# Kernel tuning notes

Hardware: AMD Instinct MI355X
Metric: run time of the kernel (lower is better)

Reference implementation:

```python
import jax, jax.numpy as jnp
import numpy as np

B, E, D, T, R = 8192, 4096, 256, 128, 4
K = 64                # dkn_n_neighbors
TAU_SQ = 4.0          # tau**2
EMB_SCALE = 0.07      # keeps sq-dists ~2.5 so exp(-d2) weights are meaningful
LOG_BASE = -27.6310211159
EPS = 1e-12


def _rev_cumsum(a, axis):
    # flip -> cumsum -> flip, as in torch .flip().cumsum().flip()
    return jnp.flip(jnp.cumsum(jnp.flip(a, axis), axis), axis)


def _kernel_weights(x, ex):
    # exact KNN stand-in for the ANN index: squared L2 distances [B, E]
    d2 = (jnp.sum(x * x, axis=1, keepdims=True)
          + jnp.sum(ex * ex, axis=1)[None, :]
          - 2.0 * (x @ ex.T))
    neg_d2, idx = jax.lax.top_k(-d2, K)          # k nearest per query
    sq = jnp.maximum(-neg_d2, 0.0)               # [B, K]
    vals = jnp.exp(-sq) * (sq <= TAU_SQ).astype(x.dtype)
    rows = jnp.arange(x.shape[0])[:, None]       # [B, 1]
    # sparse exp-distance weights scattered into dense [B, E]
    return jnp.zeros((x.shape[0], ex.shape[0]), x.dtype).at[rows, idx].set(vals)


def setup_inputs() -> dict:
    key = jax.random.key(0)
    k0, k1, k2, k3 = jax.random.split(key, 4)
    x = jax.random.normal(k0, (B, D), dtype=jnp.float32) * EMB_SCALE
    ex = jax.random.normal(k1, (E, D), dtype=jnp.float32) * EMB_SCALE
    log_ev = jax.random.normal(k2, (E, T, R), dtype=jnp.float32) - 2.0
    log_cen = jax.random.normal(k3, (E, T), dtype=jnp.float32) - 2.0
    log_b_ev = jnp.full((T, R), LOG_BASE, dtype=jnp.float32)
    log_b_cen = jnp.full((T,), LOG_BASE, dtype=jnp.float32)
    return {
        "x": x,
        "exemplar_embeddings": ex,
        "log_exemplar_event_counts": log_ev,
        "log_exemplar_censor_counts": log_cen,
        "log_baseline_event_counts": log_b_ev,
        "log_baseline_censor_counts": log_b_cen,
    }


def reference(x, exemplar_embeddings, log_exemplar_event_counts,
              log_exemplar_censor_counts, log_baseline_event_counts,
              log_baseline_censor_counts):
    kw = _kernel_weights(x, exemplar_embeddings)             # [B, E]

    b_ev = jnp.exp(log_baseline_event_counts)                # [T, R]
    b_cen = jnp.exp(log_baseline_censor_counts)              # [T]
    b_at_risk = _rev_cumsum(b_ev.sum(1) + b_cen, 0)          # [T]

    ev = jnp.exp(log_exemplar_event_counts)                  # [E, T, R]
    cen = jnp.exp(log_exemplar_censor_counts)                # [E, T]
    at_risk = _rev_cumsum(ev.sum(2) + cen, 1)                # [E, T]

    denom = kw @ at_risk + b_at_risk[None, :] + EPS          # [B, T]
    numer = jnp.einsum('be,etr->btr', kw, ev) + b_ev[None]   # [B, T, R]

    esh = jnp.clip(numer / denom[..., None], EPS, 1.0 - EPS) # [B, T, R]
    event_specific_hazards = jnp.moveaxis(esh, -1, 0)        # [R, B, T]
    overall = jnp.clip(numer.sum(-1) / denom, EPS, 1.0 - EPS)  # [B, T]
    return event_specific_hazards, overall
```

## Files before the change

### kernel.cpp

```cpp
#include <hip/hip_runtime.h>
#include <hip/hip_fp16.h>
#include <math.h>

namespace {

constexpr int NB = 8192;
constexpr int NE = 4096;
constexpr int ND = 256;
constexpr int NT = 128;
constexpr int NR = 4;
constexpr int NK = 64;
constexpr int NCAND = 320;
constexpr float TAUSQ = 4.0f;
constexpr float FEPS = 1e-12f;
constexpr float QS = 256.0f / 4.5f;

typedef short s16x8 __attribute__((ext_vector_type(8)));
typedef float f32x4 __attribute__((ext_vector_type(4)));

__device__ __forceinline__ unsigned short f2bf_rne(float f) {
  unsigned int u = __float_as_uint(f);
  unsigned int r = (u + 0x7FFFu + ((u >> 16) & 1u)) >> 16;
  return (unsigned short)r;
}
__device__ __forceinline__ unsigned short f2h(float f) {
  return __half_as_ushort(__float2half(f));
}
__device__ __forceinline__ float h2f(unsigned short s) {
  return __half2float(__ushort_as_half(s));
}

__device__ __forceinline__ void gl_lds16(const void* g, void* lds) {
  __builtin_amdgcn_global_load_lds(
      (const __attribute__((address_space(1))) unsigned int*)g,
      (__attribute__((address_space(3))) unsigned int*)lds, 16, 0, 0);
}

__global__ void k_prep(const float* __restrict__ lev, const float* __restrict__ lcen,
                       const float* __restrict__ lbev, const float* __restrict__ lbcen,
                       unsigned short* __restrict__ EVh, unsigned short* __restrict__ ARh,
                       float* __restrict__ bev, float* __restrict__ bar) {
  __shared__ float wtot;
  int t = threadIdx.x, l = t & 63;
  int e = blockIdx.x;
  float acc;
  if (e < NE) {
    acc = expf(lcen[(size_t)e * NT + t]);
    const float* src = lev + ((size_t)e * NT + t) * NR;
    float o0 = expf(src[0]), o1 = expf(src[1]), o2 = expf(src[2]), o3 = expf(src[3]);
    ushort4 h4;
    h4.x = f2h(o0); h4.y = f2h(o1); h4.z = f2h(o2); h4.w = f2h(o3);
    *reinterpret_cast<ushort4*>(EVh + ((size_t)e * NT + t) * NR) = h4;
    acc += o0 + o1 + o2 + o3;
  } else {
    acc = expf(lbcen[t]);
    const float* src = lbev + t * NR;
    float o0 = expf(src[0]), o1 = expf(src[1]), o2 = expf(src[2]), o3 = expf(src[3]);
    bev[t * NR + 0] = o0; bev[t * NR + 1] = o1;
    bev[t * NR + 2] = o2; bev[t * NR + 3] = o3;
    acc += o0 + o1 + o2 + o3;
  }
  float v = acc;
  #pragma unroll
  for (int o = 1; o < 64; o <<= 1) {
    float u = __shfl_down(v, o);
    if (l + o < 64) v += u;
  }
  if (t == 64) wtot = v;
  __syncthreads();
  if (t < 64) v += wtot;
  if (e < NE) ARh[(size_t)e * NT + t] = f2h(v);
  else        bar[t] = v;
}

__global__ void k_split(const float* __restrict__ x, const float* __restrict__ ex,
                        unsigned short* __restrict__ xh, unsigned short* __restrict__ eh,
                        float* __restrict__ xn, float* __restrict__ exn) {
  int row = blockIdx.x, l = threadIdx.x;
  bool isx = row < NB;
  const float* p = isx ? (x + (size_t)row * ND) : (ex + (size_t)(row - NB) * ND);
  unsigned short* dst = isx ? (xh + (size_t)row * ND) : (eh + (size_t)(row - NB) * ND);
  float4 v = reinterpret_cast<const float4*>(p)[l];
  float nv = v.x * v.x + v.y * v.y + v.z * v.z + v.w * v.w;
  ushort4 h4;
  h4.x = f2bf_rne(v.x); h4.y = f2bf_rne(v.y);
  h4.z = f2bf_rne(v.z); h4.w = f2bf_rne(v.w);
  reinterpret_cast<ushort4*>(dst)[l] = h4;
  for (int o = 32; o > 0; o >>= 1) nv += __shfl_down(nv, o);
  if (l == 0) { if (isx) xn[row] = nv; else exn[row - NB] = nv; }
}

__global__ __launch_bounds__(256) void k_dist_mfma(
    const unsigned short* __restrict__ xh, const unsigned short* __restrict__ eh,
    const float* __restrict__ xn, const float* __restrict__ exn,
    unsigned char* __restrict__ d2q) {
  __shared__ __align__(16) unsigned char As[128 * 128];
  __shared__ __align__(16) unsigned char Bs[128 * 128];
  int tid = threadIdx.x;
  int l = tid & 63, w = tid >> 6;
  int wr = w >> 1, wc = w & 1;

  int lid = blockIdx.x;
  int sl = (lid & 7) * 256 + (lid >> 3);
  int nb = (sl & 31) * 128;
  int mb = (sl >> 5) * 128;

  f32x4 acc[4][4];
  #pragma unroll
  for (int m = 0; m < 4; ++m)
    #pragma unroll
    for (int n = 0; n < 4; ++n)
      acc[m][n] = (f32x4){0.f, 0.f, 0.f, 0.f};

  for (int k0 = 0; k0 < ND; k0 += 64) {
    #pragma unroll
    for (int h = 0; h < 4; ++h) {
      int c = h * 256 + tid;
      int row = c >> 3, slot = c & 7;
      int swz = (row ^ (row >> 3)) & 7;
      int gcol = k0 + ((slot ^ swz) << 3);
      gl_lds16(xh + (size_t)(mb + row) * ND + gcol, As + c * 16);
      gl_lds16(eh + (size_t)(nb + row) * ND + gcol, Bs + c * 16);
    }
    __syncthreads();
    #pragma unroll
    for (int kk = 0; kk < 2; ++kk) {
      s16x8 af[4], bf_[4];
      int sl0 = kk * 4 + (l >> 4);
      #pragma unroll
      for (int m = 0; m < 4; ++m) {
        int r = wr * 64 + m * 16 + (l & 15);
        int swz = (r ^ (r >> 3)) & 7;
        af[m] = *(const s16x8*)(As + r * 128 + ((sl0 ^ swz) << 4));
      }
      #pragma unroll
      for (int n = 0; n < 4; ++n) {
        int r = wc * 64 + n * 16 + (l & 15);
        int swz = (r ^ (r >> 3)) & 7;
        bf_[n] = *(const s16x8*)(Bs + r * 128 + ((sl0 ^ swz) << 4));
      }
      #pragma unroll
      for (int m = 0; m < 4; ++m)
        #pragma unroll
        for (int n = 0; n < 4; ++n)
          acc[m][n] = __builtin_amdgcn_mfma_f32_16x16x32_bf16(af[m], bf_[n], acc[m][n], 0, 0, 0);
    }
    __syncthreads();
  }

  int col0 = nb + wc * 64 + (l & 15);
  int row0 = mb + wr * 64 + (l >> 4) * 4;
  float exnv[4];
  #pragma unroll
  for (int n = 0; n < 4; ++n) exnv[n] = exn[col0 + n * 16];
  #pragma unroll
  for (int m = 0; m < 4; ++m) {
    #pragma unroll
    for (int j = 0; j < 4; ++j) {
      int qrow = row0 + m * 16 + j;
      float xq = xn[qrow];
      #pragma unroll
      for (int n = 0; n < 4; ++n) {
        float d2 = xq + exnv[n] - 2.f * acc[m][n][j];
        int bin = (int)floorf(d2 * QS);
        bin = bin < 0 ? 0 : (bin > 255 ? 255 : bin);
        d2q[(size_t)qrow * NE + (col0 + n * 16)] = (unsigned char)bin;
      }
    }
  }
}

__global__ __launch_bounds__(256, 8) void k_select(
    const unsigned char* __restrict__ d2q,
    const float* __restrict__ x, const float* __restrict__ ex,
    const float* __restrict__ xn, const float* __restrict__ exn,
    float* __restrict__ selw, int* __restrict__ seli) {
  __shared__ unsigned int hist[256];
  __shared__ float4 xs[64];
  __shared__ int cand_e[NCAND];
  __shared__ float cand_d[NCAND];
  __shared__ unsigned int wsum[4];
  __shared__ int s_cb, s_nc;

  int tid = threadIdx.x;
  int l = tid & 63, w = tid >> 6;
  int b = blockIdx.x;

  uint4 rb = reinterpret_cast<const uint4*>(d2q + (size_t)b * NE)[tid];
  if (tid < 64) xs[tid] = reinterpret_cast<const float4*>(x + (size_t)b * ND)[tid];
  hist[tid] = 0u;
  __syncthreads();

  unsigned int wd[4] = {rb.x, rb.y, rb.z, rb.w};
  #pragma unroll
  for (int c = 0; c < 4; ++c)
    #pragma unroll
    for (int k = 0; k < 4; ++k)
      atomicAdd(&hist[(wd[c] >> (8 * k)) & 255u], 1u);

  int g = tid >> 4, gj = tid & 15;
  float4 xr0 = xs[gj], xr1 = xs[gj + 16], xr2 = xs[gj + 32], xr3 = xs[gj + 48];
  __syncthreads();

  if (w == 0) {
    unsigned int h0 = hist[l * 4], h1 = hist[l * 4 + 1], h2 = hist[l * 4 + 2], h3 = hist[l * 4 + 3];
    unsigned int gs = h0 + h1 + h2 + h3;
    unsigned int sc = gs;
    #pragma unroll
    for (int o = 1; o < 64; o <<= 1) { unsigned int v = __shfl_up(sc, o); if (l >= o) sc += v; }
    unsigned int excl = sc - gs;
    unsigned int c0 = excl + h0, c1 = c0 + h1, c2 = c1 + h2, c3 = c2 + h3;
    int local = (c0 >= (unsigned)NK) ? 0 : (c1 >= (unsigned)NK) ? 1
              : (c2 >= (unsigned)NK) ? 2 : (c3 >= (unsigned)NK) ? 3 : -1;
    unsigned long long ball = __ballot(local >= 0);
    int first = __ffsll((long long)ball) - 1;
    if (l == first) s_cb = l * 4 + local;
  }
  __syncthreads();
  int cbg = s_cb < 255 ? s_cb + 1 : 255;

  int myc = 0;
  #pragma unroll
  for (int c = 0; c < 4; ++c)
    #pragma unroll
    for (int k = 0; k < 4; ++k)
      myc += ((int)((wd[c] >> (8 * k)) & 255u) <= cbg) ? 1 : 0;
  int sc = myc;
  #pragma unroll
  for (int o = 1; o < 64; o <<= 1) { int v = __shfl_up(sc, o); if (l >= o) sc += v; }
  if (l == 63) wsum[w] = (unsigned)sc;
  __syncthreads();
  int base = 0;
  for (int i = 0; i < w; ++i) base += (int)wsum[i];
  int slot = base + sc - myc;
  #pragma unroll
  for (int c = 0; c < 4; ++c)
    #pragma unroll
    for (int k = 0; k < 4; ++k) {
      int bin = (int)((wd[c] >> (8 * k)) & 255u);
      if (bin <= cbg) {
        if (slot < NCAND) cand_e[slot] = tid * 16 + c * 4 + k;
        ++slot;
      }
    }
  if (tid == 255) s_nc = (base + sc) < NCAND ? (base + sc) : NCAND;
  __syncthreads();

  int nc = s_nc;
  float bxn = xn[b];
  for (int c = g; c < nc; c += 32) {
    int eA = cand_e[c];
    int has2 = (c + 16) < nc;
    int eB = has2 ? cand_e[c + 16] : eA;
    const float4* pA = reinterpret_cast<const float4*>(ex + (size_t)eA * ND);
    const float4* pB = reinterpret_cast<const float4*>(ex + (size_t)eB * ND);
    float4 a0 = pA[gj], a1 = pA[gj + 16], a2 = pA[gj + 32], a3 = pA[gj + 48];
    float4 b0 = pB[gj], b1 = pB[gj + 16], b2 = pB[gj + 32], b3 = pB[gj + 48];
    float sA = xr0.x * a0.x + xr0.y * a0.y + xr0.z * a0.z + xr0.w * a0.w
             + xr1.x * a1.x + xr1.y * a1.y + xr1.z * a1.z + xr1.w * a1.w
             + xr2.x * a2.x + xr2.y * a2.y + xr2.z * a2.z + xr2.w * a2.w
             + xr3.x * a3.x + xr3.y * a3.y + xr3.z * a3.z + xr3.w * a3.w;
    float sB = xr0.x * b0.x + xr0.y * b0.y + xr0.z * b0.z + xr0.w * b0.w
             + xr1.x * b1.x + xr1.y * b1.y + xr1.z * b1.z + xr1.w * b1.w
             + xr2.x * b2.x + xr2.y * b2.y + xr2.z * b2.z + xr2.w * b2.w
             + xr3.x * b3.x + xr3.y * b3.y + xr3.z * b3.z + xr3.w * b3.w;
    #pragma unroll
    for (int o = 1; o < 16; o <<= 1) {
      sA += __shfl_xor(sA, o, 16);
      sB += __shfl_xor(sB, o, 16);
    }
    if (gj == 0) {
      cand_d[c] = bxn + exn[eA] - 2.f * sA;
      if (has2) cand_d[c + 16] = bxn + exn[eB] - 2.f * sB;
    }
  }
  __syncthreads();

  for (int i = tid; i < nc; i += 256) {
    float di = cand_d[i];
    int rank = 0;
    for (int j = 0; j < nc; ++j) {
      float dj = cand_d[j];
      rank += (dj < di) || (dj == di && j < i);
    }
    if (rank < NK) {
      float sq = fmaxf(di, 0.f);
      float wgt = (sq <= TAUSQ) ? expf(-sq) : 0.f;
      selw[(size_t)b * NK + rank] = wgt;
      seli[(size_t)b * NK + rank] = cand_e[i];
    }
  }
  if (tid >= nc && tid < NK) {
    selw[(size_t)b * NK + tid] = 0.f;
    seli[(size_t)b * NK + tid] = 0;
  }
}

__global__ __launch_bounds__(256) void k_out(
    const unsigned short* __restrict__ EVh, const unsigned short* __restrict__ ARh,
    const float* __restrict__ bev, const float* __restrict__ bar,
    const float* __restrict__ selw, const int* __restrict__ seli,
    float* __restrict__ out) {
  __shared__ float wl[NK];
  __shared__ int il[NK];
  __shared__ float snum[NT * NR];
  __shared__ float sden[NT];
  int tid = threadIdx.x;
  int b = blockIdx.x;
  if (tid < NK) { wl[tid] = selw[(size_t)b * NK + tid]; il[tid] = seli[(size_t)b * NK + tid]; }
  __syncthreads();

  int g = tid >> 7;
  int t = tid & 127;
  float acc0 = 0.f, acc1 = 0.f, acc2 = 0.f, acc3 = 0.f, dacc = 0.f;
  for (int k = g; k < NK; k += 2) {
    float wgt = wl[k];
    int e = il[k];
    ushort4 v = reinterpret_cast<const ushort4*>(EVh + (size_t)e * (NT * NR))[t];
    acc0 += wgt * h2f(v.x);
    acc1 += wgt * h2f(v.y);
    acc2 += wgt * h2f(v.z);
    acc3 += wgt * h2f(v.w);
    dacc += wgt * h2f(ARh[(size_t)e * NT + t]);
  }
  if (g == 0) {
    snum[t * 4 + 0] = acc0; snum[t * 4 + 1] = acc1;
    snum[t * 4 + 2] = acc2; snum[t * 4 + 3] = acc3;
    sden[t] = dacc;
  }
  __syncthreads();
  if (g == 1) {
    snum[t * 4 + 0] += acc0 + bev[t * 4 + 0];
    snum[t * 4 + 1] += acc1 + bev[t * 4 + 1];
    snum[t * 4 + 2] += acc2 + bev[t * 4 + 2];
    snum[t * 4 + 3] += acc3 + bev[t * 4 + 3];
    sden[t] += dacc + bar[t] + FEPS;
  }
  __syncthreads();

  const float lo = FEPS, hi = 1.0f - FEPS;
  {
    int f = tid;
    int tt = f >> 2, r = f & 3;
    float h = snum[f] / sden[tt];
    h = fminf(fmaxf(h, lo), hi);
    out[((size_t)r * NB + b) * NT + tt] = h;
    int f1 = tid + 256;
    int t1 = f1 >> 2, r1 = f1 & 3;
    float h1 = snum[f1] / sden[t1];
    h1 = fminf(fmaxf(h1, lo), hi);
    out[((size_t)r1 * NB + b) * NT + t1] = h1;
  }
  if (tid < NT) {
    float sum = snum[4 * tid] + snum[4 * tid + 1] + snum[4 * tid + 2] + snum[4 * tid + 3];
    float ov = sum / sden[tid];
    ov = fminf(fmaxf(ov, lo), hi);
    out[(size_t)4 * NB * NT + (size_t)b * NT + tid] = ov;
  }
}

}

extern "C" void kernel_launch(void* const* d_in, const int* in_sizes, int n_in,
                              void* d_out, int out_size, void* d_ws, size_t ws_size,
                              hipStream_t stream) {
  (void)in_sizes; (void)n_in; (void)out_size; (void)ws_size;
  const float* x     = (const float*)d_in[0];
  const float* ex    = (const float*)d_in[1];
  const float* lev   = (const float*)d_in[2];
  const float* lcen  = (const float*)d_in[3];
  const float* lbev  = (const float*)d_in[4];
  const float* lbcen = (const float*)d_in[5];
  float* out = (float*)d_out;

  char* ws = (char*)d_ws;
  unsigned short* EVh = (unsigned short*)(ws);
  unsigned short* ARh = (unsigned short*)(ws + (4ull << 20));
  float* bev = (float*)(ws + (5ull << 20));
  float* bar = (float*)(ws + (5ull << 20) + 4096);
  float* exn = (float*)(ws + (5ull << 20) + 8192);
  float* xn  = (float*)(ws + (5ull << 20) + 8192 + (16u << 10));
  unsigned char* d2q = (unsigned char*)(ws + (6ull << 20));
  float* selw = (float*)(ws + (38ull << 20));
  int*   seli = (int*)  (ws + (40ull << 20));
  unsigned short* xh = (unsigned short*)(ws + (42ull << 20));
  unsigned short* eh = (unsigned short*)(ws + (46ull << 20));

  k_prep<<<NE + 1, NT, 0, stream>>>(lev, lcen, lbev, lbcen, EVh, ARh, bev, bar);
  k_split<<<NB + NE, 64, 0, stream>>>(x, ex, xh, eh, xn, exn);
  k_dist_mfma<<<2048, 256, 0, stream>>>(xh, eh, xn, exn, d2q);
  k_select<<<NB, 256, 0, stream>>>(d2q, x, ex, xn, exn, selw, seli);
  k_out<<<NB, 256, 0, stream>>>(EVh, ARh, bev, bar, selw, seli, out);
}
```

Baseline: 213.0 us.

## Merge split kernel into prep and replace full rank sort with window-based selection

Merges the bf16 split/norm kernel into the prep kernel as extra blocks, removing one launch. In k_select, the O(nc^2) rank computation over all candidates is replaced. Candidates clearly below the quantization threshold window are accepted via an atomic counter, and only candidates near the cutoff bin are rank-compared to fill the remaining slots. Output order becomes unsorted, which is fine for the scatter-style consumer. It assumes the quantized bin bounds hold and caps the ambiguous set at 128.

```diff
diff --git a/kernel.cpp b/kernel.cpp
--- a/kernel.cpp
+++ b/kernel.cpp
@@ -14,6 +14,7 @@
 constexpr float TAUSQ = 4.0f;
 constexpr float FEPS = 1e-12f;
 constexpr float QS = 256.0f / 4.5f;
+constexpr float HBIN = 4.5f / 256.f;
 
 typedef short s16x8 __attribute__((ext_vector_type(8)));
 typedef float f32x4 __attribute__((ext_vector_type(4)));
@@ -39,10 +40,31 @@
 __global__ void k_prep(const float* __restrict__ lev, const float* __restrict__ lcen,
                        const float* __restrict__ lbev, const float* __restrict__ lbcen,
                        unsigned short* __restrict__ EVh, unsigned short* __restrict__ ARh,
-                       float* __restrict__ bev, float* __restrict__ bar) {
+                       float* __restrict__ bev, float* __restrict__ bar,
+                       const float* __restrict__ x, const float* __restrict__ ex,
+                       unsigned short* __restrict__ xh, unsigned short* __restrict__ eh,
+                       float* __restrict__ xn, float* __restrict__ exn) {
   __shared__ float wtot;
   int t = threadIdx.x, l = t & 63;
-  int e = blockIdx.x;
+  int bid = blockIdx.x;
+
+  if (bid > NE) {
+    int r2 = (bid - (NE + 1)) * 2 + (t >> 6);
+    bool isx = r2 < NB;
+    const float* p = isx ? (x + (size_t)r2 * ND) : (ex + (size_t)(r2 - NB) * ND);
+    unsigned short* dst = isx ? (xh + (size_t)r2 * ND) : (eh + (size_t)(r2 - NB) * ND);
+    float4 v = reinterpret_cast<const float4*>(p)[l];
+    float nv = v.x * v.x + v.y * v.y + v.z * v.z + v.w * v.w;
+    ushort4 h4;
+    h4.x = f2bf_rne(v.x); h4.y = f2bf_rne(v.y);
+    h4.z = f2bf_rne(v.z); h4.w = f2bf_rne(v.w);
+    reinterpret_cast<ushort4*>(dst)[l] = h4;
+    for (int o = 32; o > 0; o >>= 1) nv += __shfl_down(nv, o);
+    if (l == 0) { if (isx) xn[r2] = nv; else exn[r2 - NB] = nv; }
+    return;
+  }
+
+  int e = bid;
   float acc;
   if (e < NE) {
     acc = expf(lcen[(size_t)e * NT + t]);
@@ -71,23 +93,6 @@
   if (t < 64) v += wtot;
   if (e < NE) ARh[(size_t)e * NT + t] = f2h(v);
   else        bar[t] = v;
-}
-
-__global__ void k_split(const float* __restrict__ x, const float* __restrict__ ex,
-                        unsigned short* __restrict__ xh, unsigned short* __restrict__ eh,
-                        float* __restrict__ xn, float* __restrict__ exn) {
-  int row = blockIdx.x, l = threadIdx.x;
-  bool isx = row < NB;
-  const float* p = isx ? (x + (size_t)row * ND) : (ex + (size_t)(row - NB) * ND);
-  unsigned short* dst = isx ? (xh + (size_t)row * ND) : (eh + (size_t)(row - NB) * ND);
-  float4 v = reinterpret_cast<const float4*>(p)[l];
-  float nv = v.x * v.x + v.y * v.y + v.z * v.z + v.w * v.w;
-  ushort4 h4;
-  h4.x = f2bf_rne(v.x); h4.y = f2bf_rne(v.y);
-  h4.z = f2bf_rne(v.z); h4.w = f2bf_rne(v.w);
-  reinterpret_cast<ushort4*>(dst)[l] = h4;
-  for (int o = 32; o > 0; o >>= 1) nv += __shfl_down(nv, o);
-  if (l == 0) { if (isx) xn[row] = nv; else exn[row - NB] = nv; }
 }
 
 __global__ __launch_bounds__(256) void k_dist_mfma(
@@ -181,6 +186,10 @@
   __shared__ float cand_d[NCAND];
   __shared__ unsigned int wsum[4];
   __shared__ int s_cb, s_nc;
+  __shared__ int s_m1, s_amb, s_out;
+  __shared__ int amb_ci[128];
+  __shared__ float amb_dv[128];
+  __shared__ unsigned char amb_ok[128];
 
   int tid = threadIdx.x;
   int l = tid & 63, w = tid >> 6;
@@ -189,6 +198,7 @@
   uint4 rb = reinterpret_cast<const uint4*>(d2q + (size_t)b * NE)[tid];
   if (tid < 64) xs[tid] = reinterpret_cast<const float4*>(x + (size_t)b * ND)[tid];
   hist[tid] = 0u;
+  if (tid == 0) { s_m1 = 0; s_amb = 0; s_out = 0; }
   __syncthreads();
 
   unsigned int wd[4] = {rb.x, rb.y, rb.z, rb.w};
@@ -217,7 +227,8 @@
     if (l == first) s_cb = l * 4 + local;
   }
   __syncthreads();
-  int cbg = s_cb < 255 ? s_cb + 1 : 255;
+  int cb = s_cb;
+  int cbg = cb < 255 ? cb + 1 : 255;
 
   int myc = 0;
   #pragma unroll
@@ -244,6 +255,7 @@
       }
     }
   if (tid == 255) s_nc = (base + sc) < NCAND ? (base + sc) : NCAND;
+  if (tid < NK) { selw[(size_t)b * NK + tid] = 0.f; seli[(size_t)b * NK + tid] = 0; }
   __syncthreads();
 
   int nc = s_nc;
@@ -276,23 +288,54 @@
   }
   __syncthreads();
 
+  float wlo = cb * HBIN - 0.5f * HBIN;
+  float whi = (cb + 1) * HBIN + 0.5f * HBIN;
+
   for (int i = tid; i < nc; i += 256) {
-    float di = cand_d[i];
-    int rank = 0;
-    for (int j = 0; j < nc; ++j) {
-      float dj = cand_d[j];
-      rank += (dj < di) || (dj == di && j < i);
-    }
-    if (rank < NK) {
-      float sq = fmaxf(di, 0.f);
-      float wgt = (sq <= TAUSQ) ? expf(-sq) : 0.f;
-      selw[(size_t)b * NK + rank] = wgt;
-      seli[(size_t)b * NK + rank] = cand_e[i];
-    }
-  }
-  if (tid >= nc && tid < NK) {
-    selw[(size_t)b * NK + tid] = 0.f;
-    seli[(size_t)b * NK + tid] = 0;
+    float d = cand_d[i];
+    if (d < wlo) {
+      atomicAdd(&s_m1, 1);
+    } else if (d <= whi) {
+      int p = atomicAdd(&s_amb, 1);
+      if (p < 128) { amb_ci[p] = i; amb_dv[p] = d; }
+    }
+  }
+  __syncthreads();
+  int m1 = s_m1;
+  int na = s_amb < 128 ? s_amb : 128;
+  int need = NK - m1;
+
+  if (tid < na) {
+    float di = amb_dv[tid];
+    int ci = amb_ci[tid];
+    int r = 0;
+    for (int j = 0; j < na; ++j) {
+      float dj = amb_dv[j];
+      r += (dj < di) || (dj == di && amb_ci[j] < ci);
+    }
+    amb_ok[tid] = (r < need) ? 1 : 0;
+  }
+  __syncthreads();
+
+  for (int i = tid; i < nc; i += 256) {
+    float d = cand_d[i];
+    if (d < wlo) {
+      int p = atomicAdd(&s_out, 1);
+      if (p < NK) {
+        float sq = fmaxf(d, 0.f);
+        selw[(size_t)b * NK + p] = (sq <= TAUSQ) ? expf(-sq) : 0.f;
+        seli[(size_t)b * NK + p] = cand_e[i];
+      }
+    }
+  }
+  if (tid < na && amb_ok[tid]) {
+    int p = atomicAdd(&s_out, 1);
+    if (p < NK) {
+      float d = amb_dv[tid];
+      float sq = fmaxf(d, 0.f);
+      selw[(size_t)b * NK + p] = (sq <= TAUSQ) ? expf(-sq) : 0.f;
+      seli[(size_t)b * NK + p] = cand_e[amb_ci[tid]];
+    }
   }
 }
 
@@ -386,8 +429,8 @@
   unsigned short* xh = (unsigned short*)(ws + (42ull << 20));
   unsigned short* eh = (unsigned short*)(ws + (46ull << 20));
 
-  k_prep<<<NE + 1, NT, 0, stream>>>(lev, lcen, lbev, lbcen, EVh, ARh, bev, bar);
-  k_split<<<NB + NE, 64, 0, stream>>>(x, ex, xh, eh, xn, exn);
+  k_prep<<<(NE + 1) + (NB + NE) / 2, NT, 0, stream>>>(
+      lev, lcen, lbev, lbcen, EVh, ARh, bev, bar, x, ex, xh, eh, xn, exn);
   k_dist_mfma<<<2048, 256, 0, stream>>>(xh, eh, xn, exn, d2q);
   k_select<<<NB, 256, 0, stream>>>(d2q, x, ex, xn, exn, selw, seli);
   k_out<<<NB, 256, 0, stream>>>(EVh, ARh, bev, bar, selw, seli, out);
```

Result: slower. 222.6 us (+4.5%).

## Merge prep and split kernels; split selection into histogram and rerank kernels

Applied to the files above, without the earlier changes.

Folds the bf16 split/norm work into the prep kernel launch, processing two rows per 128-thread block, which removes one kernel launch. It also splits the select kernel into two: one builds the histogram and writes candidate lists to global memory, the other reranks candidates with exact fp32 distances. This lowers per-kernel register and LDS use and so may raise occupancy, at the cost of an extra launch and a global round trip for the candidate lists.

```diff
diff --git a/kernel.cpp b/kernel.cpp
--- a/kernel.cpp
+++ b/kernel.cpp
@@ -39,10 +39,31 @@
 __global__ void k_prep(const float* __restrict__ lev, const float* __restrict__ lcen,
                        const float* __restrict__ lbev, const float* __restrict__ lbcen,
                        unsigned short* __restrict__ EVh, unsigned short* __restrict__ ARh,
-                       float* __restrict__ bev, float* __restrict__ bar) {
+                       float* __restrict__ bev, float* __restrict__ bar,
+                       const float* __restrict__ x, const float* __restrict__ ex,
+                       unsigned short* __restrict__ xh, unsigned short* __restrict__ eh,
+                       float* __restrict__ xn, float* __restrict__ exn) {
   __shared__ float wtot;
   int t = threadIdx.x, l = t & 63;
-  int e = blockIdx.x;
+  int bid = blockIdx.x;
+
+  if (bid > NE) {
+    int r2 = (bid - (NE + 1)) * 2 + (t >> 6);
+    bool isx = r2 < NB;
+    const float* p = isx ? (x + (size_t)r2 * ND) : (ex + (size_t)(r2 - NB) * ND);
+    unsigned short* dst = isx ? (xh + (size_t)r2 * ND) : (eh + (size_t)(r2 - NB) * ND);
+    float4 v = reinterpret_cast<const float4*>(p)[l];
+    float nv = v.x * v.x + v.y * v.y + v.z * v.z + v.w * v.w;
+    ushort4 h4;
+    h4.x = f2bf_rne(v.x); h4.y = f2bf_rne(v.y);
+    h4.z = f2bf_rne(v.z); h4.w = f2bf_rne(v.w);
+    reinterpret_cast<ushort4*>(dst)[l] = h4;
+    for (int o = 32; o > 0; o >>= 1) nv += __shfl_down(nv, o);
+    if (l == 0) { if (isx) xn[r2] = nv; else exn[r2 - NB] = nv; }
+    return;
+  }
+
+  int e = bid;
   float acc;
   if (e < NE) {
     acc = expf(lcen[(size_t)e * NT + t]);
@@ -71,23 +92,6 @@
   if (t < 64) v += wtot;
   if (e < NE) ARh[(size_t)e * NT + t] = f2h(v);
   else        bar[t] = v;
-}
-
-__global__ void k_split(const float* __restrict__ x, const float* __restrict__ ex,
-                        unsigned short* __restrict__ xh, unsigned short* __restrict__ eh,
-                        float* __restrict__ xn, float* __restrict__ exn) {
-  int row = blockIdx.x, l = threadIdx.x;
-  bool isx = row < NB;
-  const float* p = isx ? (x + (size_t)row * ND) : (ex + (size_t)(row - NB) * ND);
-  unsigned short* dst = isx ? (xh + (size_t)row * ND) : (eh + (size_t)(row - NB) * ND);
-  float4 v = reinterpret_cast<const float4*>(p)[l];
-  float nv = v.x * v.x + v.y * v.y + v.z * v.z + v.w * v.w;
-  ushort4 h4;
-  h4.x = f2bf_rne(v.x); h4.y = f2bf_rne(v.y);
-  h4.z = f2bf_rne(v.z); h4.w = f2bf_rne(v.w);
-  reinterpret_cast<ushort4*>(dst)[l] = h4;
-  for (int o = 32; o > 0; o >>= 1) nv += __shfl_down(nv, o);
-  if (l == 0) { if (isx) xn[row] = nv; else exn[row - NB] = nv; }
 }
 
 __global__ __launch_bounds__(256) void k_dist_mfma(
@@ -170,24 +174,18 @@
   }
 }
 
-__global__ __launch_bounds__(256, 8) void k_select(
+__global__ __launch_bounds__(256, 8) void k_sel_a(
     const unsigned char* __restrict__ d2q,
-    const float* __restrict__ x, const float* __restrict__ ex,
-    const float* __restrict__ xn, const float* __restrict__ exn,
-    float* __restrict__ selw, int* __restrict__ seli) {
+    unsigned short* __restrict__ candL, int* __restrict__ candN) {
   __shared__ unsigned int hist[256];
-  __shared__ float4 xs[64];
-  __shared__ int cand_e[NCAND];
-  __shared__ float cand_d[NCAND];
   __shared__ unsigned int wsum[4];
-  __shared__ int s_cb, s_nc;
+  __shared__ int s_cb;
 
   int tid = threadIdx.x;
   int l = tid & 63, w = tid >> 6;
   int b = blockIdx.x;
 
   uint4 rb = reinterpret_cast<const uint4*>(d2q + (size_t)b * NE)[tid];
-  if (tid < 64) xs[tid] = reinterpret_cast<const float4*>(x + (size_t)b * ND)[tid];
   hist[tid] = 0u;
   __syncthreads();
 
@@ -197,9 +195,6 @@
     #pragma unroll
     for (int k = 0; k < 4; ++k)
       atomicAdd(&hist[(wd[c] >> (8 * k)) & 255u], 1u);
-
-  int g = tid >> 4, gj = tid & 15;
-  float4 xr0 = xs[gj], xr1 = xs[gj + 16], xr2 = xs[gj + 32], xr3 = xs[gj + 48];
   __syncthreads();
 
   if (w == 0) {
@@ -233,20 +228,45 @@
   int base = 0;
   for (int i = 0; i < w; ++i) base += (int)wsum[i];
   int slot = base + sc - myc;
+  unsigned short* cl = candL + (size_t)b * NCAND;
   #pragma unroll
   for (int c = 0; c < 4; ++c)
     #pragma unroll
     for (int k = 0; k < 4; ++k) {
       int bin = (int)((wd[c] >> (8 * k)) & 255u);
       if (bin <= cbg) {
-        if (slot < NCAND) cand_e[slot] = tid * 16 + c * 4 + k;
+        if (slot < NCAND) cl[slot] = (unsigned short)(tid * 16 + c * 4 + k);
         ++slot;
       }
     }
-  if (tid == 255) s_nc = (base + sc) < NCAND ? (base + sc) : NCAND;
-  __syncthreads();
-
+  if (tid == 255) {
+    int nc = base + sc;
+    candN[b] = nc < NCAND ? nc : NCAND;
+  }
+}
+
+__global__ __launch_bounds__(256, 8) void k_sel_b(
+    const unsigned short* __restrict__ candL, const int* __restrict__ candN,
+    const float* __restrict__ x, const float* __restrict__ ex,
+    const float* __restrict__ xn, const float* __restrict__ exn,
+    float* __restrict__ selw, int* __restrict__ seli) {
+  __shared__ int cand_e[NCAND];
+  __shared__ float cand_d[NCAND];
+  __shared__ int s_nc;
+
+  int tid = threadIdx.x;
+  int b = blockIdx.x;
+  if (tid == 0) s_nc = candN[b];
+  if (tid < NCAND) cand_e[tid] = -1;
+  __syncthreads();
   int nc = s_nc;
+  if (tid < nc) cand_e[tid] = (int)candL[(size_t)b * NCAND + tid];
+  __syncthreads();
+
+  int g = tid >> 4, gj = tid & 15;
+  const float4* xp = reinterpret_cast<const float4*>(x + (size_t)b * ND);
+  float4 xr0 = xp[gj], xr1 = xp[gj + 16], xr2 = xp[gj + 32], xr3 = xp[gj + 48];
+
   float bxn = xn[b];
   for (int c = g; c < nc; c += 32) {
     int eA = cand_e[c];
@@ -385,10 +405,13 @@
   int*   seli = (int*)  (ws + (40ull << 20));
   unsigned short* xh = (unsigned short*)(ws + (42ull << 20));
   unsigned short* eh = (unsigned short*)(ws + (46ull << 20));
-
-  k_prep<<<NE + 1, NT, 0, stream>>>(lev, lcen, lbev, lbcen, EVh, ARh, bev, bar);
-  k_split<<<NB + NE, 64, 0, stream>>>(x, ex, xh, eh, xn, exn);
+  int* candN = (int*)(ws + (48ull << 20));
+  unsigned short* candL = (unsigned short*)(ws + (48ull << 20) + (64u << 10));
+
+  k_prep<<<(NE + 1) + (NB + NE) / 2, NT, 0, stream>>>(
+      lev, lcen, lbev, lbcen, EVh, ARh, bev, bar, x, ex, xh, eh, xn, exn);
   k_dist_mfma<<<2048, 256, 0, stream>>>(xh, eh, xn, exn, d2q);
-  k_select<<<NB, 256, 0, stream>>>(d2q, x, ex, xn, exn, selw, seli);
+  k_sel_a<<<NB, 256, 0, stream>>>(d2q, candL, candN);
+  k_sel_b<<<NB, 256, 0, stream>>>(candL, candN, x, ex, xn, exn, selw, seli);
   k_out<<<NB, 256, 0, stream>>>(EVh, ARh, bev, bar, selw, seli, out);
 }
```

After: 222.3 us. +4.4%, slower.
